# Performance work log

Hardware: AMD Instinct MI355X
Metric: run time of the kernel (lower is better)

The kernel has to match this reference:

```python
import jax, jax.numpy as jnp
import numpy as np

N = 10000          # num mesh vertices
NSPEC = 64         # spectral basis size (V[:, :64], D[:64, :])
K = 6              # Chebyshev order
IN_DESC = 352      # input descriptor dims (SHOT)
OUT_DESC = 256     # output descriptor dims
EPS = 1e-3


def _bn(x, g, b):
    # BatchNorm1d over the node (batch) dim, training-mode batch statistics
    m = x.mean(axis=0)
    v = x.var(axis=0)
    return (x - m) * jax.lax.rsqrt(v + EPS) * g + b


def _cheb(x, V, D, eigs, W, b):
    # Spectral Laplacian apply: L z = V @ (eigs * (D @ z)); cost O(N*64*C)
    def L(z):
        return V @ (eigs[:, None] * (D @ z))
    T_prev, T_cur = x, L(x)
    out = T_prev @ W[0] + T_cur @ W[1]
    for k in range(2, K):
        T_next = 2.0 * L(T_cur) - T_prev
        out = out + T_next @ W[k]
        T_prev, T_cur = T_cur, T_next
    return out + b


def setup_inputs() -> dict:
    key = jax.random.key(0)
    ks = jax.random.split(key, 12)
    s = lambda fan_in: 1.0 / np.sqrt(fan_in)
    return {
        "x": jax.random.normal(ks[0], (N, IN_DESC), jnp.float32),
        "V": jax.random.normal(ks[1], (N, NSPEC), jnp.float32) * (1.0 / np.sqrt(N)),
        "D": jax.random.normal(ks[2], (NSPEC, N), jnp.float32) * (1.0 / np.sqrt(N)),
        "eigs": jax.random.uniform(ks[3], (NSPEC,), jnp.float32),
        "fc1_w": jax.random.normal(ks[4], (IN_DESC, 64), jnp.float32) * s(IN_DESC),
        "fc1_b": jnp.zeros((64,), jnp.float32),
        "bf1_g": jnp.ones((64,), jnp.float32),
        "bf1_b": jnp.zeros((64,), jnp.float32),
        "W1": jax.random.normal(ks[5], (K, 64, 64), jnp.float32) * s(64 * K),
        "cb1": jnp.zeros((64,), jnp.float32),
        "b1_g": jnp.ones((64,), jnp.float32),
        "b1_b": jnp.zeros((64,), jnp.float32),
        "W2": jax.random.normal(ks[6], (K, 64, 64), jnp.float32) * s(64 * K),
        "cb2": jnp.zeros((64,), jnp.float32),
        "b2_g": jnp.ones((64,), jnp.float32),
        "b2_b": jnp.zeros((64,), jnp.float32),
        "W3": jax.random.normal(ks[7], (K, 64, 128), jnp.float32) * s(64 * K),
        "cb3": jnp.zeros((128,), jnp.float32),
        "b3_g": jnp.ones((128,), jnp.float32),
        "b3_b": jnp.zeros((128,), jnp.float32),
        "fc2_w": jax.random.normal(ks[8], (128, OUT_DESC), jnp.float32) * s(128),
        "fc2_b": jnp.zeros((OUT_DESC,), jnp.float32),
        "bf2_g": jnp.ones((OUT_DESC,), jnp.float32),
        "bf2_b": jnp.zeros((OUT_DESC,), jnp.float32),
        "fc3_w": jax.random.normal(ks[9], (OUT_DESC, N), jnp.float32) * s(OUT_DESC),
        "fc3_b": jnp.zeros((N,), jnp.float32),
    }


def reference(x, V, D, eigs, fc1_w, fc1_b, bf1_g, bf1_b,
              W1, cb1, b1_g, b1_b, W2, cb2, b2_g, b2_b,
              W3, cb3, b3_g, b3_b, fc2_w, fc2_b, bf2_g, bf2_b,
              fc3_w, fc3_b):
    h = jax.nn.relu(_bn(x @ fc1_w + fc1_b, bf1_g, bf1_b))
    h = jax.nn.relu(_bn(_cheb(h, V, D, eigs, W1, cb1), b1_g, b1_b))
    h = jax.nn.relu(_bn(_cheb(h, V, D, eigs, W2, cb2), b2_g, b2_b))
    h = jax.nn.relu(_bn(_cheb(h, V, D, eigs, W3, cb3), b3_g, b3_b))
    desc = jax.nn.relu(_bn(h @ fc2_w + fc2_b, bf2_g, bf2_b))
    logits = desc @ fc3_w + fc3_b  # [N, N] correspondence logits
    return jax.nn.log_softmax(logits, axis=1), desc
```

## Files before the change

### kernel.cpp

```cpp
#include <hip/hip_runtime.h>
#include <hip/hip_bf16.h>

#define NV 10000
#define PADM 10112

typedef __attribute__((ext_vector_type(8))) short bf16x8;
typedef __attribute__((ext_vector_type(4))) float f32x4;

__device__ __forceinline__ void g2l16(const void* g, void* l) {
  __builtin_amdgcn_global_load_lds((__attribute__((address_space(1))) void*)(void*)g,
                                   (__attribute__((address_space(3))) void*)l, 16, 0, 0);
}

__global__ __launch_bounds__(256) void gemm_f32(
    const float* __restrict__ A1, int K1, const float* __restrict__ A2, int K2,
    const float* __restrict__ B, const float* __restrict__ bias,
    float* __restrict__ Y, float* __restrict__ stats, int N)
{
  __shared__ float As[64][36];
  __shared__ float Bs[32][68];
  const int tid = threadIdx.x;
  const int row0 = blockIdx.x * 64;
  const int n0 = blockIdx.y * 64;
  const int tr = tid >> 4, tc = tid & 15;
  const int Ktot = K1 + K2;
  float acc[4][4];
#pragma unroll
  for (int i = 0; i < 4; ++i)
#pragma unroll
    for (int j = 0; j < 4; ++j) acc[i][j] = 0.f;

  for (int k0 = 0; k0 < Ktot; k0 += 32) {
    const float* Ap; int lda, ka;
    if (k0 < K1) { Ap = A1; lda = K1; ka = k0; }
    else         { Ap = A2; lda = K2; ka = k0 - K1; }
    __syncthreads();
    {
      int r = tid >> 3, seg = tid & 7;
#pragma unroll
      for (int h = 0; h < 2; ++h) {
        int rr = r + h * 32;
        int gr = row0 + rr; if (gr > NV - 1) gr = NV - 1;
        float4 v = *(const float4*)(Ap + (size_t)gr * lda + ka + seg * 4);
        *(float4*)&As[rr][seg * 4] = v;
      }
      int kr = tid >> 4, cseg = tid & 15;
#pragma unroll
      for (int h = 0; h < 2; ++h) {
        int kk = kr + h * 16;
        float4 v = *(const float4*)(B + (size_t)(k0 + kk) * N + n0 + cseg * 4);
        *(float4*)&Bs[kk][cseg * 4] = v;
      }
    }
    __syncthreads();
#pragma unroll 8
    for (int kk = 0; kk < 32; ++kk) {
      float4 bv = *(const float4*)&Bs[kk][tc * 4];
#pragma unroll
      for (int i = 0; i < 4; ++i) {
        float a = As[tr * 4 + i][kk];
        acc[i][0] = fmaf(a, bv.x, acc[i][0]);
        acc[i][1] = fmaf(a, bv.y, acc[i][1]);
        acc[i][2] = fmaf(a, bv.z, acc[i][2]);
        acc[i][3] = fmaf(a, bv.w, acc[i][3]);
      }
    }
  }
  float bvv[4];
#pragma unroll
  for (int j = 0; j < 4; ++j) bvv[j] = bias[n0 + tc * 4 + j];
  float cs[4] = {0.f, 0.f, 0.f, 0.f}, cq[4] = {0.f, 0.f, 0.f, 0.f};
#pragma unroll
  for (int i = 0; i < 4; ++i) {
    int gr = row0 + tr * 4 + i;
    bool ok = gr < NV;
    float o[4];
#pragma unroll
    for (int j = 0; j < 4; ++j) {
      float v = acc[i][j] + bvv[j];
      o[j] = v;
      if (ok) { cs[j] += v; cq[j] += v * v; }
    }
    if (ok) *(float4*)(Y + (size_t)gr * N + n0 + tc * 4) = make_float4(o[0], o[1], o[2], o[3]);
  }
  __syncthreads();
  float* red = &As[0][0];
#pragma unroll
  for (int j = 0; j < 4; ++j) {
    red[tr * 68 + tc * 4 + j] = cs[j];
    red[1088 + tr * 68 + tc * 4 + j] = cq[j];
  }
  __syncthreads();
  if (tid < 64) {
    float s = 0.f, q = 0.f;
#pragma unroll
    for (int t = 0; t < 16; ++t) { s += red[t * 68 + tid]; q += red[1088 + t * 68 + tid]; }
    atomicAdd(&stats[n0 + tid], s);
    atomicAdd(&stats[256 + n0 + tid], q);
  }
}

__global__ __launch_bounds__(256) void bn_relu(
    const float* __restrict__ Y, const float* __restrict__ stats,
    const float* __restrict__ g, const float* __restrict__ bt,
    float* __restrict__ out, unsigned short* __restrict__ outb, int C)
{
  int gid = blockIdx.x * 256 + threadIdx.x;
  int total = NV * (C >> 2);
  if (gid >= total) return;
  int c = (gid * 4) % C;
  float4 y = *(const float4*)(Y + (size_t)gid * 4);
  float vy[4] = {y.x, y.y, y.z, y.w};
  float o[4];
#pragma unroll
  for (int j = 0; j < 4; ++j) {
    int cc = c + j;
    float mean = stats[cc] * 1e-4f;
    float var  = stats[256 + cc] * 1e-4f - mean * mean;
    float sc = rsqrtf(var + 1e-3f) * g[cc];
    float sh = bt[cc] - mean * sc;
    o[j] = fmaxf(0.f, fmaf(vy[j], sc, sh));
  }
  *(float4*)(out + (size_t)gid * 4) = make_float4(o[0], o[1], o[2], o[3]);
  if (outb != nullptr) {
    unsigned short u[4];
#pragma unroll
    for (int j = 0; j < 4; ++j) {
      __hip_bfloat16 h = __float2bfloat16(o[j]);
      u[j] = *(unsigned short*)&h;
    }
    *(ushort2*)(outb + (size_t)gid * 4)     = make_ushort2(u[0], u[1]);
    *(ushort2*)(outb + (size_t)gid * 4 + 2) = make_ushort2(u[2], u[3]);
  }
}

__global__ __launch_bounds__(256) void dx_atomic(
    const float* __restrict__ Dm, const float* __restrict__ X, float* __restrict__ outm)
{
  __shared__ float Ds[64][40];
  __shared__ float Xs[40][64];
  const int tid = threadIdx.x;
  const int k0 = blockIdx.x * 40;
  const float* xp = X + (size_t)k0 * 64;
  for (int i = tid; i < 2560; i += 256) ((float*)Xs)[i] = xp[i];
  {
    int r = tid >> 2, qq = tid & 3;
#pragma unroll
    for (int m = 0; m < 10; ++m) Ds[r][qq + 4 * m] = Dm[(size_t)r * NV + k0 + qq + 4 * m];
  }
  __syncthreads();
  const int j = tid & 63, ig = tid >> 6;
  float acc[16];
#pragma unroll
  for (int ii = 0; ii < 16; ++ii) acc[ii] = 0.f;
  for (int k = 0; k < 40; ++k) {
    float xv = Xs[k][j];
#pragma unroll
    for (int ii = 0; ii < 16; ++ii) acc[ii] = fmaf(Ds[ig * 16 + ii][k], xv, acc[ii]);
  }
  float* op = outm + (size_t)ig * 1024 + j;
#pragma unroll
  for (int ii = 0; ii < 16; ++ii) atomicAdd(&op[ii * 64], acc[ii]);
}

__global__ __launch_bounds__(256) void chainA(
    const float* __restrict__ DVm, const float* __restrict__ eigs, float* __restrict__ Acat)
{
  __shared__ float DVL[64][68];
  __shared__ float AL[3][64][68];
  __shared__ float ev[64];
  const int tid = threadIdx.x;
  for (int i = tid; i < 4096; i += 256) DVL[i >> 6][i & 63] = DVm[i];
  if (tid < 64) ev[tid] = eigs[tid];
  __syncthreads();
  for (int i = tid; i < 4096; i += 256) {
    int r = i >> 6, c = i & 63;
    AL[0][r][c] = 0.f;
    float v = (r == c) ? ev[r] : 0.f;
    AL[1][r][c] = v;
    Acat[i] = v;
  }
  __syncthreads();
  const int tr = tid >> 4, tc = tid & 15;
  float aK[4]; aK[0] = 0.f; aK[1] = -1.f; aK[2] = 0.f; aK[3] = 1.f;
  for (int k = 1; k <= 4; ++k) {
    int cur = k % 3, prv = (k - 1) % 3, nxt = (k + 1) % 3;
    float g4[4][4];
#pragma unroll
    for (int ii = 0; ii < 4; ++ii)
#pragma unroll
      for (int jj = 0; jj < 4; ++jj) g4[ii][jj] = 0.f;
    for (int p = 0; p < 64; ++p) {
      float4 av = *(const float4*)&AL[cur][p][tc * 4];
#pragma unroll
      for (int ii = 0; ii < 4; ++ii) {
        float dv = DVL[tr * 4 + ii][p];
        g4[ii][0] = fmaf(dv, av.x, g4[ii][0]);
        g4[ii][1] = fmaf(dv, av.y, g4[ii][1]);
        g4[ii][2] = fmaf(dv, av.z, g4[ii][2]);
        g4[ii][3] = fmaf(dv, av.w, g4[ii][3]);
      }
    }
    float ak = aK[k - 1];
#pragma unroll
    for (int ii = 0; ii < 4; ++ii) {
      int i = tr * 4 + ii;
#pragma unroll
      for (int jj = 0; jj < 4; ++jj) {
        int j = tc * 4 + jj;
        float gg = g4[ii][jj] + ((i == j) ? ak : 0.f);
        float v = 2.f * ev[i] * gg - AL[prv][i][j];
        AL[nxt][i][j] = v;
        Acat[(size_t)k * 4096 + i * 64 + j] = v;
      }
    }
    __syncthreads();
  }
}

__global__ __launch_bounds__(256) void mcat_k(
    const float* __restrict__ Acat, const float* __restrict__ S0, float* __restrict__ Mcat)
{
  __shared__ float AL[64][68];
  __shared__ float SL[64][68];
  const int kb = blockIdx.x;
  const int tid = threadIdx.x;
  for (int i = tid; i < 4096; i += 256) {
    AL[i >> 6][i & 63] = Acat[(size_t)kb * 4096 + i];
    SL[i >> 6][i & 63] = S0[i];
  }
  __syncthreads();
  const int tr = tid >> 4, tc = tid & 15;
  float g4[4][4];
#pragma unroll
  for (int ii = 0; ii < 4; ++ii)
#pragma unroll
    for (int jj = 0; jj < 4; ++jj) g4[ii][jj] = 0.f;
  for (int p = 0; p < 64; ++p) {
    float4 sv = *(const float4*)&SL[p][tc * 4];
#pragma unroll
    for (int ii = 0; ii < 4; ++ii) {
      float a = AL[tr * 4 + ii][p];
      g4[ii][0] = fmaf(a, sv.x, g4[ii][0]);
      g4[ii][1] = fmaf(a, sv.y, g4[ii][1]);
      g4[ii][2] = fmaf(a, sv.z, g4[ii][2]);
      g4[ii][3] = fmaf(a, sv.w, g4[ii][3]);
    }
  }
#pragma unroll
  for (int ii = 0; ii < 4; ++ii)
#pragma unroll
    for (int jj = 0; jj < 4; ++jj)
      Mcat[(size_t)(tr * 4 + ii) * 320 + kb * 64 + tc * 4 + jj] = g4[ii][jj];
}

__global__ __launch_bounds__(256) void bc_k(
    const float* __restrict__ W, const float* __restrict__ Mcat,
    float* __restrict__ Bc, int Cout)
{
  int e = blockIdx.x * 256 + threadIdx.x;
  int row = e / Cout, j = e - row * Cout;
  if (row < 64) {
    Bc[e] = W[row * Cout + j] - W[128 * Cout + row * Cout + j] + W[256 * Cout + row * Cout + j];
  } else {
    int i = row - 64;
    const float* wc = W + 64 * Cout + j;
    const float* mr = Mcat + (size_t)i * 320;
    float s = 0.f;
#pragma unroll 8
    for (int qq = 0; qq < 320; ++qq) s = fmaf(mr[qq], wc[(size_t)qq * Cout], s);
    Bc[e] = s;
  }
}

__global__ __launch_bounds__(256) void cast_transpose_w(
    const float* __restrict__ w, unsigned short* __restrict__ wT)
{
  __shared__ float tile[32][33];
  int n0 = blockIdx.x * 32, k0 = blockIdx.y * 32;
  int t = threadIdx.x;
  int rr = t >> 5, cc = t & 31;
#pragma unroll
  for (int p = 0; p < 4; ++p) {
    int k = k0 + rr + p * 8, n = n0 + cc;
    tile[rr + p * 8][cc] = (n < NV) ? w[(size_t)k * NV + n] : 0.f;
  }
  __syncthreads();
#pragma unroll
  for (int p = 0; p < 4; ++p) {
    int n = n0 + rr + p * 8, k = k0 + cc;
    __hip_bfloat16 h = __float2bfloat16(tile[cc][rr + p * 8]);
    wT[(size_t)n * 256 + k] = *(unsigned short*)&h;
  }
}

template<bool WRITE>
__global__ __launch_bounds__(256) void fc3_k(
    const unsigned short* __restrict__ A, const unsigned short* __restrict__ Bt,
    const float* __restrict__ bias, float* __restrict__ rowsum,
    float* __restrict__ out)
{
  __shared__ unsigned short As[2][128 * 64];
  __shared__ unsigned short Bs[2][128 * 64];
  const int tid = threadIdx.x;
  const int wv = tid >> 6, lane = tid & 63;
  const int row0 = blockIdx.x * 128, col0 = blockIdx.y * 128;
  const int wr = wv >> 1, wc = wv & 1;
  f32x4 acc[4][4];
#pragma unroll
  for (int i = 0; i < 4; ++i)
#pragma unroll
    for (int j = 0; j < 4; ++j)
#pragma unroll
      for (int e = 0; e < 4; ++e) acc[i][j][e] = 0.f;

  const int rs = wv * 8 + (lane >> 3);
  const int csg = (lane & 7) * 8;
  const int gsg = ((lane & 7) ^ (lane >> 3)) * 8;
  const int swz = (lane & 7) << 3;
  const unsigned short* Ag = A  + (size_t)(row0 + rs) * 256 + gsg;
  const unsigned short* Bg = Bt + (size_t)(col0 + rs) * 256 + gsg;
  const int mbase = wr * 64 + (lane & 15);
  const int nbase = wc * 64 + (lane & 15);

#pragma unroll
  for (int i = 0; i < 4; ++i) {
    g2l16(Ag + (size_t)(i * 32) * 256, &As[0][(i * 32 + rs) * 64 + csg]);
    g2l16(Bg + (size_t)(i * 32) * 256, &Bs[0][(i * 32 + rs) * 64 + csg]);
  }
#pragma unroll
  for (int t = 0; t < 4; ++t) {
    __syncthreads();
    if (t < 3) {
      const int b = (t + 1) & 1, kt = (t + 1) * 64;
#pragma unroll
      for (int i = 0; i < 4; ++i) {
        g2l16(Ag + (size_t)(i * 32) * 256 + kt, &As[b][(i * 32 + rs) * 64 + csg]);
        g2l16(Bg + (size_t)(i * 32) * 256 + kt, &Bs[b][(i * 32 + rs) * 64 + csg]);
      }
    }
    __builtin_amdgcn_s_setprio(1);
#pragma unroll
    for (int kk = 0; kk < 2; ++kk) {
      const int kb = (kk * 32 + (lane >> 4) * 8) ^ swz;
      bf16x8 af[4], bf[4];
#pragma unroll
      for (int mi = 0; mi < 4; ++mi) af[mi] = *(const bf16x8*)&As[t & 1][(mbase + mi * 16) * 64 + kb];
#pragma unroll
      for (int ni = 0; ni < 4; ++ni) bf[ni] = *(const bf16x8*)&Bs[t & 1][(nbase + ni * 16) * 64 + kb];
#pragma unroll
      for (int mi = 0; mi < 4; ++mi)
#pragma unroll
        for (int ni = 0; ni < 4; ++ni)
          acc[mi][ni] = __builtin_amdgcn_mfma_f32_16x16x32_bf16(af[mi], bf[ni], acc[mi][ni], 0, 0, 0);
    }
    __builtin_amdgcn_s_setprio(0);
  }
  const int q = lane >> 4, cl = lane & 15;
#pragma unroll
  for (int mi = 0; mi < 4; ++mi) {
#pragma unroll
    for (int r = 0; r < 4; ++r) {
      int grow = row0 + wr * 64 + mi * 16 + q * 4 + r;
      if (WRITE) {
        if (grow < NV) {
          float l = 20.f + __logf(rowsum[grow]);
#pragma unroll
          for (int ni = 0; ni < 4; ++ni) {
            int gcol = col0 + wc * 64 + ni * 16 + cl;
            if (gcol < NV)
              out[(size_t)grow * NV + gcol] = acc[mi][ni][r] + bias[gcol] - l;
          }
        }
      } else {
        float ps = 0.f;
        if (grow < NV) {
#pragma unroll
          for (int ni = 0; ni < 4; ++ni) {
            int gcol = col0 + wc * 64 + ni * 16 + cl;
            if (gcol < NV) ps += __expf(acc[mi][ni][r] + bias[gcol] - 20.f);
          }
        }
#pragma unroll
        for (int s = 1; s < 16; s <<= 1) ps += __shfl_xor(ps, s, 64);
        if (cl == 0 && grow < NV) atomicAdd(&rowsum[grow], ps);
      }
    }
  }
}

extern "C" void kernel_launch(void* const* d_in, const int* in_sizes, int n_in,
                              void* d_out, int out_size, void* d_ws, size_t ws_size,
                              hipStream_t stream)
{
  const float* x     = (const float*)d_in[0];
  const float* V     = (const float*)d_in[1];
  const float* D     = (const float*)d_in[2];
  const float* eigs  = (const float*)d_in[3];
  const float* fc1_w = (const float*)d_in[4];
  const float* fc1_b = (const float*)d_in[5];
  const float* bf1_g = (const float*)d_in[6];
  const float* bf1_b = (const float*)d_in[7];
  const float* W1    = (const float*)d_in[8];
  const float* cb1   = (const float*)d_in[9];
  const float* b1_g  = (const float*)d_in[10];
  const float* b1_b  = (const float*)d_in[11];
  const float* W2    = (const float*)d_in[12];
  const float* cb2   = (const float*)d_in[13];
  const float* b2_g  = (const float*)d_in[14];
  const float* b2_b  = (const float*)d_in[15];
  const float* W3    = (const float*)d_in[16];
  const float* cb3   = (const float*)d_in[17];
  const float* b3_g  = (const float*)d_in[18];
  const float* b3_b  = (const float*)d_in[19];
  const float* fc2_w = (const float*)d_in[20];
  const float* fc2_b = (const float*)d_in[21];
  const float* bf2_g = (const float*)d_in[22];
  const float* bf2_b = (const float*)d_in[23];
  const float* fc3_w = (const float*)d_in[24];
  const float* fc3_b = (const float*)d_in[25];
  (void)in_sizes; (void)n_in; (void)out_size;

  float* ws = (float*)d_ws;
  float* rowsum = ws;
  float* stats  = ws + 10000;
  float* DVm    = ws + 12560;
  float* S0a    = ws + 16656;
  float* S0b    = ws + 20752;
  float* S0c    = ws + 24848;
  float* Acat   = ws + 28944;
  float* Mcat   = ws + 49424;
  float* Bc     = ws + 69904;
  float* Ybuf   = ws + 86288;
  float* actA   = ws + 2646288;
  float* actB   = ws + 3286288;
  float* h3     = ws + 3926288;
  unsigned short* descb = (unsigned short*)(ws + 5206288);
  unsigned short* wT    = (unsigned short*)(ws + 6500624);
  if (ws_size < (size_t)7794960 * 4) return;

  float* out_lsm  = (float*)d_out;
  float* out_desc = out_lsm + (size_t)100000000;

  hipMemsetAsync(ws, 0, 28944 * sizeof(float), stream);
  hipMemsetAsync(descb + (size_t)NV * 256, 0, (size_t)(PADM - NV) * 256 * 2, stream);

  cast_transpose_w<<<dim3(316, 8), 256, 0, stream>>>(fc3_w, wT);

  dx_atomic<<<250, 256, 0, stream>>>(D, V, DVm);
  chainA<<<1, 256, 0, stream>>>(DVm, eigs, Acat);

  gemm_f32<<<dim3(157, 1), 256, 0, stream>>>(x, 352, nullptr, 0, fc1_w, fc1_b,
                                             Ybuf, stats + 0 * 512, 64);
  bn_relu<<<625, 256, 0, stream>>>(Ybuf, stats + 0 * 512, bf1_g, bf1_b, actA, nullptr, 64);

  dx_atomic<<<250, 256, 0, stream>>>(D, actA, S0a);
  mcat_k<<<5, 256, 0, stream>>>(Acat, S0a, Mcat);
  bc_k<<<32, 256, 0, stream>>>(W1, Mcat, Bc, 64);
  gemm_f32<<<dim3(157, 1), 256, 0, stream>>>(actA, 64, V, 64, Bc, cb1,
                                             Ybuf, stats + 1 * 512, 64);
  bn_relu<<<625, 256, 0, stream>>>(Ybuf, stats + 1 * 512, b1_g, b1_b, actB, nullptr, 64);

  dx_atomic<<<250, 256, 0, stream>>>(D, actB, S0b);
  mcat_k<<<5, 256, 0, stream>>>(Acat, S0b, Mcat);
  bc_k<<<32, 256, 0, stream>>>(W2, Mcat, Bc, 64);
  gemm_f32<<<dim3(157, 1), 256, 0, stream>>>(actB, 64, V, 64, Bc, cb2,
                                             Ybuf, stats + 2 * 512, 64);
  bn_relu<<<625, 256, 0, stream>>>(Ybuf, stats + 2 * 512, b2_g, b2_b, actA, nullptr, 64);

  dx_atomic<<<250, 256, 0, stream>>>(D, actA, S0c);
  mcat_k<<<5, 256, 0, stream>>>(Acat, S0c, Mcat);
  bc_k<<<64, 256, 0, stream>>>(W3, Mcat, Bc, 128);
  gemm_f32<<<dim3(157, 2), 256, 0, stream>>>(actA, 64, V, 64, Bc, cb3,
                                             Ybuf, stats + 3 * 512, 128);
  bn_relu<<<1250, 256, 0, stream>>>(Ybuf, stats + 3 * 512, b3_g, b3_b, h3, nullptr, 128);

  gemm_f32<<<dim3(157, 4), 256, 0, stream>>>(h3, 128, nullptr, 0, fc2_w, fc2_b,
                                             Ybuf, stats + 4 * 512, 256);
  bn_relu<<<2500, 256, 0, stream>>>(Ybuf, stats + 4 * 512, bf2_g, bf2_b,
                                    out_desc, descb, 256);

  fc3_k<false><<<dim3(79, 79), 256, 0, stream>>>(descb, wT, fc3_b, rowsum, nullptr);
  fc3_k<true><<<dim3(79, 79), 256, 0, stream>>>(descb, wT, fc3_b, rowsum, out_lsm);
}
```

Baseline: 1.156 ms.

## Remap fc3 tiles per XCD and drop LDS double buffering

The fc3 GEMM moves from a 2D grid to a 1D grid of 6320 blocks. Each block's index is remapped so that every XCD (bid & 7) owns a contiguous band of 10 row tiles and walks across the column tiles, which should improve L2 reuse of the A rows within each XCD. The LDS tiles become single-buffered, with an explicit vmcnt(0) wait and barrier before each k-step. This halves shared memory and may raise occupancy, but global loads no longer overlap with the MFMA work.

```diff
diff --git a/kernel.cpp b/kernel.cpp
--- a/kernel.cpp
+++ b/kernel.cpp
@@ -300,11 +300,18 @@
     const float* __restrict__ bias, float* __restrict__ rowsum,
     float* __restrict__ out)
 {
-  __shared__ unsigned short As[2][128 * 64];
-  __shared__ unsigned short Bs[2][128 * 64];
+  __shared__ unsigned short As[128 * 64];
+  __shared__ unsigned short Bs[128 * 64];
+  const int bid = blockIdx.x;
+  const int xcd = bid & 7;
+  const int s   = bid >> 3;
+  const int col_t = s / 10;
+  const int row_t = xcd * 10 + (s - col_t * 10);
+  const int row0 = row_t * 128, col0 = col_t * 128;
+  if (row0 >= NV) return;
+
   const int tid = threadIdx.x;
   const int wv = tid >> 6, lane = tid & 63;
-  const int row0 = blockIdx.x * 128, col0 = blockIdx.y * 128;
   const int wr = wv >> 1, wc = wv & 1;
   f32x4 acc[4][4];
 #pragma unroll
@@ -323,31 +330,24 @@
   const int mbase = wr * 64 + (lane & 15);
   const int nbase = wc * 64 + (lane & 15);
 
-#pragma unroll
-  for (int i = 0; i < 4; ++i) {
-    g2l16(Ag + (size_t)(i * 32) * 256, &As[0][(i * 32 + rs) * 64 + csg]);
-    g2l16(Bg + (size_t)(i * 32) * 256, &Bs[0][(i * 32 + rs) * 64 + csg]);
-  }
-#pragma unroll
-  for (int t = 0; t < 4; ++t) {
+  for (int k0 = 0; k0 < 256; k0 += 64) {
     __syncthreads();
-    if (t < 3) {
-      const int b = (t + 1) & 1, kt = (t + 1) * 64;
-#pragma unroll
-      for (int i = 0; i < 4; ++i) {
-        g2l16(Ag + (size_t)(i * 32) * 256 + kt, &As[b][(i * 32 + rs) * 64 + csg]);
-        g2l16(Bg + (size_t)(i * 32) * 256 + kt, &Bs[b][(i * 32 + rs) * 64 + csg]);
-      }
-    }
+#pragma unroll
+    for (int i = 0; i < 4; ++i) {
+      g2l16(Ag + (size_t)(i * 32) * 256 + k0, &As[(i * 32 + rs) * 64 + csg]);
+      g2l16(Bg + (size_t)(i * 32) * 256 + k0, &Bs[(i * 32 + rs) * 64 + csg]);
+    }
+    asm volatile("s_waitcnt vmcnt(0)" ::: "memory");
+    __syncthreads();
     __builtin_amdgcn_s_setprio(1);
 #pragma unroll
     for (int kk = 0; kk < 2; ++kk) {
       const int kb = (kk * 32 + (lane >> 4) * 8) ^ swz;
       bf16x8 af[4], bf[4];
 #pragma unroll
-      for (int mi = 0; mi < 4; ++mi) af[mi] = *(const bf16x8*)&As[t & 1][(mbase + mi * 16) * 64 + kb];
-#pragma unroll
-      for (int ni = 0; ni < 4; ++ni) bf[ni] = *(const bf16x8*)&Bs[t & 1][(nbase + ni * 16) * 64 + kb];
+      for (int mi = 0; mi < 4; ++mi) af[mi] = *(const bf16x8*)&As[(mbase + mi * 16) * 64 + kb];
+#pragma unroll
+      for (int ni = 0; ni < 4; ++ni) bf[ni] = *(const bf16x8*)&Bs[(nbase + ni * 16) * 64 + kb];
 #pragma unroll
       for (int mi = 0; mi < 4; ++mi)
 #pragma unroll
@@ -382,7 +382,7 @@
           }
         }
 #pragma unroll
-        for (int s = 1; s < 16; s <<= 1) ps += __shfl_xor(ps, s, 64);
+        for (int sh = 1; sh < 16; sh <<= 1) ps += __shfl_xor(ps, sh, 64);
         if (cl == 0 && grow < NV) atomicAdd(&rowsum[grow], ps);
       }
     }
@@ -480,6 +480,6 @@
   bn_relu<<<2500, 256, 0, stream>>>(Ybuf, stats + 4 * 512, bf2_g, bf2_b,
                                     out_desc, descb, 256);
 
-  fc3_k<false><<<dim3(79, 79), 256, 0, stream>>>(descb, wT, fc3_b, rowsum, nullptr);
-  fc3_k<true><<<dim3(79, 79), 256, 0, stream>>>(descb, wT, fc3_b, rowsum, out_lsm);
-}
+  fc3_k<false><<<6320, 256, 0, stream>>>(descb, wT, fc3_b, rowsum, nullptr);
+  fc3_k<true><<<6320, 256, 0, stream>>>(descb, wT, fc3_b, rowsum, out_lsm);
+}
```

After: 1.016 ms. 1.14x faster.
